# Optimization experiments

Measured on AMD Instinct MI355X. Metric: run time of the kernel, lower is better.

The kernel has to match this reference:

```python
import jax, jax.numpy as jnp
import numpy as np

N_NODES = 100000
N_EDGES = 3200000
N_GRAPHS = 64
NUM_CLASSES = 40


def _pointnet_layer(h, pos, src, dst, w1, b1, w2, b2):
    # message: mlp(concat([h_j, pos_j - pos_i])) for each edge (j=src, i=dst)
    edge_feat = jnp.concatenate([h[src], pos[src] - pos[dst]], axis=-1)  # [E, Cin+3]
    m = jnp.maximum(edge_feat @ w1 + b1, 0.0) @ w2 + b2                  # [E, Cout]
    # scatter-max aggregation to destination nodes
    agg = jax.ops.segment_max(m, dst, num_segments=N_NODES)             # [N, Cout]
    # nodes with no incoming edges get -inf from segment_max; PyG fills 0
    return jnp.where(jnp.isfinite(agg), agg, 0.0)


def setup_inputs() -> dict:
    key = jax.random.key(0)
    ks = jax.random.split(key, 12)
    pos = jax.random.normal(ks[0], (N_NODES, 3), dtype=jnp.float32)
    edge_index = jax.random.randint(ks[1], (2, N_EDGES), 0, N_NODES, dtype=jnp.int64 if jax.config.jax_enable_x64 else jnp.int32)
    batch = jnp.sort(jax.random.randint(ks[2], (N_NODES,), 0, N_GRAPHS, dtype=jnp.int32))
    s = 0.1
    params = {
        'w1a': jax.random.normal(ks[3], (6, 32), dtype=jnp.float32) * s,
        'b1a': jnp.zeros((32,), dtype=jnp.float32),
        'w2a': jax.random.normal(ks[4], (32, 32), dtype=jnp.float32) * s,
        'b2a': jnp.zeros((32,), dtype=jnp.float32),
        'w1b': jax.random.normal(ks[5], (35, 32), dtype=jnp.float32) * s,
        'b1b': jnp.zeros((32,), dtype=jnp.float32),
        'w2b': jax.random.normal(ks[6], (32, 32), dtype=jnp.float32) * s,
        'b2b': jnp.zeros((32,), dtype=jnp.float32),
        'wc': jax.random.normal(ks[7], (32, NUM_CLASSES), dtype=jnp.float32) * s,
        'bc': jnp.zeros((NUM_CLASSES,), dtype=jnp.float32),
    }
    return {'pos': pos, 'edge_index': edge_index, 'batch': batch, **params}


def reference(pos, edge_index, batch, w1a, b1a, w2a, b2a, w1b, b1b, w2b, b2b, wc, bc):
    src, dst = edge_index[0], edge_index[1]
    h = _pointnet_layer(pos, pos, src, dst, w1a, b1a, w2a, b2a)  # conv1: 3 -> 32
    h = jnp.maximum(h, 0.0)
    h = _pointnet_layer(h, pos, src, dst, w1b, b1b, w2b, b2b)    # conv2: 32 -> 32
    h = jnp.maximum(h, 0.0)
    g = jax.ops.segment_max(h, batch, num_segments=N_GRAPHS)     # global max pool [G, 32]
    g = jnp.where(jnp.isfinite(g), g, 0.0)
    return g @ wc + bc                                           # [G, num_classes]
```

## Files before the change

### kernel.cpp

```cpp
#include <hip/hip_runtime.h>
#include <hip/hip_fp16.h>

#define N_NODES 100000
#define N_EDGES 3200000
#define N_GRAPHS 64
#define NUM_CLASSES 40
#define DEG_BINS 512


__global__ void hist_kernel(const int* __restrict__ dst, int* __restrict__ cnt, int n_edges) {
    int idx = blockIdx.x * blockDim.x + threadIdx.x;
    int stride = gridDim.x * blockDim.x;
    for (int e = idx; e < n_edges; e += stride)
        atomicAdd(&cnt[dst[e]], 1);
}

__global__ __launch_bounds__(1024) void scan_kernel(int* __restrict__ cnt_cursor,
                                                    int* __restrict__ row_start,
                                                    int n_nodes) {
    const int T = 1024;
    int t = threadIdx.x;
    int chunk = (n_nodes + T - 1) / T;
    int s = t * chunk;
    int e = min(s + chunk, n_nodes);
    int sum = 0;
    for (int i = s; i < e; ++i) sum += cnt_cursor[i];
    __shared__ int tmp[T];
    tmp[t] = sum;
    __syncthreads();
    for (int off = 1; off < T; off <<= 1) {
        int v = (t >= off) ? tmp[t - off] : 0;
        __syncthreads();
        tmp[t] += v;
        __syncthreads();
    }
    int run = tmp[t] - sum;
    for (int i = s; i < e; ++i) {
        int c = cnt_cursor[i];
        row_start[i] = run;
        cnt_cursor[i] = run;
        run += c;
    }
    if (t == T - 1) row_start[n_nodes] = run;
}

__global__ void scatter_kernel(const int* __restrict__ src, const int* __restrict__ dst,
                               int* __restrict__ cursor, int* __restrict__ col, int n_edges) {
    int idx = blockIdx.x * blockDim.x + threadIdx.x;
    int stride = gridDim.x * blockDim.x;
    for (int e = idx; e < n_edges; e += stride) {
        int p = atomicAdd(&cursor[dst[e]], 1);
        col[p] = src[e];
    }
}


__global__ void deg_hist_kernel(const int* __restrict__ row_start, int* __restrict__ dhist,
                                int n_nodes) {
    int n = blockIdx.x * blockDim.x + threadIdx.x;
    if (n >= n_nodes) return;
    int d = row_start[n + 1] - row_start[n];
    atomicAdd(&dhist[min(d, DEG_BINS - 1)], 1);
}

__global__ __launch_bounds__(DEG_BINS) void deg_scan_kernel(const int* __restrict__ dhist,
                                                            int* __restrict__ dcur) {
    __shared__ int tmp[DEG_BINS];
    int t = threadIdx.x;
    int v = dhist[t];
    tmp[t] = v;
    __syncthreads();
    for (int off = 1; off < DEG_BINS; off <<= 1) {
        int u = (t >= off) ? tmp[t - off] : 0;
        __syncthreads();
        tmp[t] += u;
        __syncthreads();
    }
    dcur[t] = tmp[t] - v;
}

__global__ void deg_perm_kernel(const int* __restrict__ row_start, int* __restrict__ dcur,
                                int* __restrict__ perm, int n_nodes) {
    int n = blockIdx.x * blockDim.x + threadIdx.x;
    if (n >= n_nodes) return;
    int d = row_start[n + 1] - row_start[n];
    int p = atomicAdd(&dcur[min(d, DEG_BINS - 1)], 1);
    perm[p] = n;
}


__global__ void pqa_kernel(const float* __restrict__ pos, const float* __restrict__ w1a,
                           const float* __restrict__ b1a,
                           __half* __restrict__ P, float* __restrict__ Q, int n_nodes) {
    __shared__ float wtop[3][32], wbot[3][32], sb1[32];
    int t = threadIdx.x;
    if (t < 32) {
        for (int c = 0; c < 3; ++c) {
            wtop[c][t] = w1a[c * 32 + t];
            wbot[c][t] = w1a[(3 + c) * 32 + t];
        }
        sb1[t] = b1a[t];
    }
    __syncthreads();
    int n = blockIdx.x * blockDim.x + t;
    if (n >= n_nodes) return;
    float px = pos[n * 3 + 0], py = pos[n * 3 + 1], pz = pos[n * 3 + 2];
    __attribute__((aligned(16))) __half hv[32];
    float qv[32];
#pragma unroll
    for (int k = 0; k < 32; ++k) {
        float wb = fmaf(px, wbot[0][k], fmaf(py, wbot[1][k], pz * wbot[2][k]));
        float wt = fmaf(px, wtop[0][k], fmaf(py, wtop[1][k], pz * wtop[2][k]));
        hv[k] = __float2half_rn(wt + wb);
        qv[k] = wb - sb1[k];
    }
    float4* Pp = (float4*)(P + (size_t)n * 32);
#pragma unroll
    for (int k = 0; k < 4; ++k) Pp[k] = *(float4*)&hv[k * 8];
    float4* Qp = (float4*)(Q + (size_t)n * 32);
#pragma unroll
    for (int k = 0; k < 8; ++k) Qp[k] = *(float4*)&qv[k * 4];
}

__global__ __launch_bounds__(256) void pqb_kernel(const float* __restrict__ pos,
                                                  const float* __restrict__ H,
                                                  const float* __restrict__ w1b,
                                                  const float* __restrict__ b1b,
                                                  __half* __restrict__ P, float* __restrict__ Q,
                                                  int n_nodes) {
    __shared__ float sw[35 * 32];
    __shared__ float sb1[32];
    for (int i = threadIdx.x; i < 35 * 32; i += blockDim.x) sw[i] = w1b[i];
    if (threadIdx.x < 32) sb1[threadIdx.x] = b1b[threadIdx.x];
    __syncthreads();
    int n = blockIdx.x * blockDim.x + threadIdx.x;
    if (n >= n_nodes) return;
    float h[32];
    const float4* Hp = (const float4*)(H + (size_t)n * 32);
#pragma unroll
    for (int k = 0; k < 8; ++k) *(float4*)&h[k * 4] = Hp[k];
    float px = pos[n * 3 + 0], py = pos[n * 3 + 1], pz = pos[n * 3 + 2];
    __attribute__((aligned(16))) __half hv[32];
    float qv[32];
#pragma unroll
    for (int k = 0; k < 32; ++k) {
        float pd = fmaf(px, sw[32 * 32 + k], fmaf(py, sw[33 * 32 + k], pz * sw[34 * 32 + k]));
        float hd = 0.f;
#pragma unroll
        for (int c = 0; c < 32; ++c) hd = fmaf(h[c], sw[c * 32 + k], hd);
        hv[k] = __float2half_rn(hd + pd);
        qv[k] = pd - sb1[k];
    }
    float4* Pp = (float4*)(P + (size_t)n * 32);
#pragma unroll
    for (int k = 0; k < 4; ++k) Pp[k] = *(float4*)&hv[k * 8];
    float4* Qp = (float4*)(Q + (size_t)n * 32);
#pragma unroll
    for (int k = 0; k < 8; ++k) Qp[k] = *(float4*)&qv[k * 4];
}


template <int S>
__device__ __forceinline__ float qb(float v) {
#if __has_builtin(__builtin_amdgcn_update_dpp)
    int iv = __float_as_int(v);
    return __int_as_float(
        __builtin_amdgcn_update_dpp(iv, iv, S * 0x55, 0xf, 0xf, false));
#else
    return __shfl(v, S, 4);
#endif
}

__device__ __forceinline__ void unpack8(float4 r, float* x) {
    const __half2* h = (const __half2*)&r;
    float2 f;
    f = __half22float2(h[0]); x[0] = f.x; x[1] = f.y;
    f = __half22float2(h[1]); x[2] = f.x; x[3] = f.y;
    f = __half22float2(h[2]); x[4] = f.x; x[5] = f.y;
    f = __half22float2(h[3]); x[6] = f.x; x[7] = f.y;
}

#define KBLOCK(S, FIRST)                                                       \
    _Pragma("unroll") for (int r = 0; r < 8; ++r) {                            \
        float wv[8];                                                           \
        const float* wr = sw2 + (S * 8 + r) * 32 + c8;                         \
        *(float4*)&wv[0] = *(const float4*)(wr);                               \
        *(float4*)&wv[4] = *(const float4*)(wr + 4);                           \
        float ya = qb<S>(xa[r]);                                               \
        float yb = qb<S>(xb[r]);                                               \
        float yc = qb<S>(xc[r]);                                               \
        float yd = qb<S>(xd[r]);                                               \
        if (FIRST && r == 0) {                                                 \
            _Pragma("unroll") for (int jl = 0; jl < 8; ++jl) {                 \
                ma[jl] = ya * wv[jl];                                          \
                mb[jl] = yb * wv[jl];                                          \
                mc[jl] = yc * wv[jl];                                          \
                md[jl] = yd * wv[jl];                                          \
            }                                                                  \
        } else {                                                               \
            _Pragma("unroll") for (int jl = 0; jl < 8; ++jl) {                 \
                ma[jl] = fmaf(ya, wv[jl], ma[jl]);                             \
                mb[jl] = fmaf(yb, wv[jl], mb[jl]);                             \
                mc[jl] = fmaf(yc, wv[jl], mc[jl]);                             \
                md[jl] = fmaf(yd, wv[jl], md[jl]);                             \
            }                                                                  \
        }                                                                      \
    }

__global__ __launch_bounds__(256, 4) void edge_kernel(const int* __restrict__ perm,
                                                      const int* __restrict__ row_start,
                                                      const int* __restrict__ col,
                                                      const __half* __restrict__ P,
                                                      const float* __restrict__ Q,
                                                      const float* __restrict__ w2,
                                                      const float* __restrict__ b2,
                                                      float* __restrict__ H, int n_nodes) {
    __shared__ float sw2[32 * 32];
    __shared__ float sb2[32];
    for (int i = threadIdx.x; i < 32 * 32; i += blockDim.x) sw2[i] = w2[i];
    if (threadIdx.x < 32) sb2[threadIdx.x] = b2[threadIdx.x];
    __syncthreads();
    int gid = (blockIdx.x * blockDim.x + threadIdx.x) >> 2;
    int c = threadIdx.x & 3;
    if (gid >= n_nodes) return;
    int n = perm[gid];
    int c8 = c * 8;

    float q[8];
    {
        const float4* Qp = (const float4*)(Q + (size_t)n * 32 + c8);
        *(float4*)&q[0] = Qp[0];
        *(float4*)&q[4] = Qp[1];
    }
    float acc[8];
#pragma unroll
    for (int j = 0; j < 8; ++j) acc[j] = -3.0e38f;

    int e0 = row_start[n], e1 = row_start[n + 1];
    for (int e = e0; e < e1; e += 4) {
        int el = e1 - 1;
        int ia = col[e];
        int ib = col[min(e + 1, el)];
        int ic = col[min(e + 2, el)];
        int id = col[min(e + 3, el)];
        float4 ra = *(const float4*)(P + (size_t)ia * 32 + c8);
        float4 rb = *(const float4*)(P + (size_t)ib * 32 + c8);
        float4 rc = *(const float4*)(P + (size_t)ic * 32 + c8);
        float4 rd = *(const float4*)(P + (size_t)id * 32 + c8);
        float xa[8], xb[8], xc[8], xd[8];
        unpack8(ra, xa);
        unpack8(rb, xb);
        unpack8(rc, xc);
        unpack8(rd, xd);
#pragma unroll
        for (int r = 0; r < 8; ++r) {
            xa[r] = fmaxf(xa[r] - q[r], 0.f);
            xb[r] = fmaxf(xb[r] - q[r], 0.f);
            xc[r] = fmaxf(xc[r] - q[r], 0.f);
            xd[r] = fmaxf(xd[r] - q[r], 0.f);
        }
        float ma[8], mb[8], mc[8], md[8];
        KBLOCK(0, true)
        KBLOCK(1, false)
        KBLOCK(2, false)
        KBLOCK(3, false)
#pragma unroll
        for (int jl = 0; jl < 8; ++jl)
            acc[jl] = fmaxf(acc[jl], fmaxf(fmaxf(ma[jl], mb[jl]), fmaxf(mc[jl], md[jl])));
    }
    float outv[8];
#pragma unroll
    for (int jl = 0; jl < 8; ++jl) outv[jl] = fmaxf(acc[jl] + sb2[c8 + jl], 0.f);
    float4* Hp = (float4*)(H + (size_t)n * 32 + c8);
    Hp[0] = *(float4*)&outv[0];
    Hp[1] = *(float4*)&outv[4];
}

__global__ __launch_bounds__(256) void pool_kernel(const float* __restrict__ H,
                                                   const int* __restrict__ batch,
                                                   float* __restrict__ gmax, int n_nodes) {
    int g = blockIdx.x;
    int lo = 0, hi = n_nodes;
    while (lo < hi) { int mid = (lo + hi) >> 1; if (batch[mid] < g) lo = mid + 1; else hi = mid; }
    int s = lo;
    lo = 0; hi = n_nodes;
    while (lo < hi) { int mid = (lo + hi) >> 1; if (batch[mid] < g + 1) lo = mid + 1; else hi = mid; }
    int e = lo;

    float acc[32];
#pragma unroll
    for (int ch = 0; ch < 32; ++ch) acc[ch] = 0.f;
    for (int n = s + threadIdx.x; n < e; n += blockDim.x) {
        const float4* Hp = (const float4*)(H + (size_t)n * 32);
#pragma unroll
        for (int k = 0; k < 8; ++k) {
            float4 v = Hp[k];
            acc[k * 4 + 0] = fmaxf(acc[k * 4 + 0], v.x);
            acc[k * 4 + 1] = fmaxf(acc[k * 4 + 1], v.y);
            acc[k * 4 + 2] = fmaxf(acc[k * 4 + 2], v.z);
            acc[k * 4 + 3] = fmaxf(acc[k * 4 + 3], v.w);
        }
    }
#pragma unroll
    for (int off = 32; off >= 1; off >>= 1)
#pragma unroll
        for (int ch = 0; ch < 32; ++ch) acc[ch] = fmaxf(acc[ch], __shfl_xor(acc[ch], off));
    __shared__ float red[4][32];
    int wid = threadIdx.x >> 6, lane = threadIdx.x & 63;
    if (lane == 0)
#pragma unroll
        for (int ch = 0; ch < 32; ++ch) red[wid][ch] = acc[ch];
    __syncthreads();
    if (threadIdx.x < 32) {
        int ch = threadIdx.x;
        float v = fmaxf(fmaxf(red[0][ch], red[1][ch]), fmaxf(red[2][ch], red[3][ch]));
        gmax[g * 32 + ch] = v;
    }
}

__global__ void classifier_kernel(const float* __restrict__ gmax, const float* __restrict__ wc,
                                  const float* __restrict__ bc, float* __restrict__ out) {
    int idx = blockIdx.x * blockDim.x + threadIdx.x;
    if (idx >= N_GRAPHS * NUM_CLASSES) return;
    int g = idx / NUM_CLASSES, c = idx % NUM_CLASSES;
    float v = bc[c];
#pragma unroll
    for (int k = 0; k < 32; ++k) v = fmaf(gmax[g * 32 + k], wc[k * NUM_CLASSES + c], v);
    out[idx] = v;
}


extern "C" void kernel_launch(void* const* d_in, const int* in_sizes, int n_in,
                              void* d_out, int out_size, void* d_ws, size_t ws_size,
                              hipStream_t stream) {
    const float* pos = (const float*)d_in[0];
    const int* ei = (const int*)d_in[1];
    const int* batch = (const int*)d_in[2];
    const float* w1a = (const float*)d_in[3];
    const float* b1a = (const float*)d_in[4];
    const float* w2a = (const float*)d_in[5];
    const float* b2a = (const float*)d_in[6];
    const float* w1b = (const float*)d_in[7];
    const float* b1b = (const float*)d_in[8];
    const float* w2b = (const float*)d_in[9];
    const float* b2b = (const float*)d_in[10];
    const float* wc = (const float*)d_in[11];
    const float* bc = (const float*)d_in[12];
    float* out = (float*)d_out;

    __half* Pbuf = (__half*)d_ws;
    float* Qbuf = (float*)d_ws + (size_t)N_NODES * 32;
    float* Hbuf = Qbuf + (size_t)N_NODES * 32;
    int* row_start = (int*)(Hbuf + (size_t)N_NODES * 32);
    int* cursor = row_start + (N_NODES + 1);
    int* col = cursor + N_NODES;
    int* perm = col + N_EDGES;
    int* dhist = perm + N_NODES;
    int* dcur = dhist + DEG_BINS;
    float* gmax = (float*)(dcur + DEG_BINS);

    const int* srcv = ei;
    const int* dstv = ei + N_EDGES;

    hipMemsetAsync(cursor, 0, N_NODES * sizeof(int), stream);
    hipMemsetAsync(dhist, 0, DEG_BINS * sizeof(int), stream);
    hist_kernel<<<2048, 256, 0, stream>>>(dstv, cursor, N_EDGES);
    scan_kernel<<<1, 1024, 0, stream>>>(cursor, row_start, N_NODES);
    scatter_kernel<<<2048, 256, 0, stream>>>(srcv, dstv, cursor, col, N_EDGES);

    int nblk = (N_NODES + 255) / 256;
    deg_hist_kernel<<<nblk, 256, 0, stream>>>(row_start, dhist, N_NODES);
    deg_scan_kernel<<<1, DEG_BINS, 0, stream>>>(dhist, dcur);
    deg_perm_kernel<<<nblk, 256, 0, stream>>>(row_start, dcur, perm, N_NODES);

    int eblk = ((N_NODES * 4) + 255) / 256;
    pqa_kernel<<<nblk, 256, 0, stream>>>(pos, w1a, b1a, Pbuf, Qbuf, N_NODES);
    edge_kernel<<<eblk, 256, 0, stream>>>(perm, row_start, col, Pbuf, Qbuf, w2a, b2a, Hbuf, N_NODES);
    pqb_kernel<<<nblk, 256, 0, stream>>>(pos, Hbuf, w1b, b1b, Pbuf, Qbuf, N_NODES);
    edge_kernel<<<eblk, 256, 0, stream>>>(perm, row_start, col, Pbuf, Qbuf, w2b, b2b, Hbuf, N_NODES);

    pool_kernel<<<N_GRAPHS, 256, 0, stream>>>(Hbuf, batch, gmax, N_NODES);
    classifier_kernel<<<(N_GRAPHS * NUM_CLASSES + 255) / 256, 256, 0, stream>>>(gmax, wc, bc, out);
}
```

Before: 2.621 ms.

## Shard edges by source range so edge gathers hit a cache-sized slice of P

Edges are bucketed into four shards by source-node range, giving a CSR per (shard, dst). Each edge-kernel block handles one shard, so its gathers of P rows come from a quarter of the node table and should get better cache locality. Per-shard partial maxima are written in fp16 and merged by a new reduce kernel that also adds the bias and applies the ReLU. The per-node Q term is now computed inside the edge kernel from pos, removing the Q buffer, in exchange for extra partial-max traffic, an extra launch, a four-times-larger scan, and fp16 rounding of the partial maxima.

```diff
diff --git a/kernel.cpp b/kernel.cpp
--- a/kernel.cpp
+++ b/kernel.cpp
@@ -6,23 +6,28 @@
 #define N_GRAPHS 64
 #define NUM_CLASSES 40
 #define DEG_BINS 512
-
-
-__global__ void hist_kernel(const int* __restrict__ dst, int* __restrict__ cnt, int n_edges) {
+#define NSH 4
+#define SHARD_N 25000
+
+
+__global__ void hist_kernel(const int* __restrict__ src, const int* __restrict__ dst,
+                            int* __restrict__ cnt, int n_edges) {
     int idx = blockIdx.x * blockDim.x + threadIdx.x;
     int stride = gridDim.x * blockDim.x;
-    for (int e = idx; e < n_edges; e += stride)
-        atomicAdd(&cnt[dst[e]], 1);
+    for (int e = idx; e < n_edges; e += stride) {
+        int s = src[e];
+        atomicAdd(&cnt[(s / SHARD_N) * N_NODES + dst[e]], 1);
+    }
 }
 
 __global__ __launch_bounds__(1024) void scan_kernel(int* __restrict__ cnt_cursor,
                                                     int* __restrict__ row_start,
-                                                    int n_nodes) {
+                                                    int n) {
     const int T = 1024;
     int t = threadIdx.x;
-    int chunk = (n_nodes + T - 1) / T;
+    int chunk = (n + T - 1) / T;
     int s = t * chunk;
-    int e = min(s + chunk, n_nodes);
+    int e = min(s + chunk, n);
     int sum = 0;
     for (int i = s; i < e; ++i) sum += cnt_cursor[i];
     __shared__ int tmp[T];
@@ -41,7 +46,7 @@
         cnt_cursor[i] = run;
         run += c;
     }
-    if (t == T - 1) row_start[n_nodes] = run;
+    if (t == T - 1) row_start[n] = run;
 }
 
 __global__ void scatter_kernel(const int* __restrict__ src, const int* __restrict__ dst,
@@ -49,18 +54,25 @@
     int idx = blockIdx.x * blockDim.x + threadIdx.x;
     int stride = gridDim.x * blockDim.x;
     for (int e = idx; e < n_edges; e += stride) {
-        int p = atomicAdd(&cursor[dst[e]], 1);
-        col[p] = src[e];
-    }
-}
-
-
-__global__ void deg_hist_kernel(const int* __restrict__ row_start, int* __restrict__ dhist,
+        int s = src[e];
+        int p = atomicAdd(&cursor[(s / SHARD_N) * N_NODES + dst[e]], 1);
+        col[p] = s;
+    }
+}
+
+
+__device__ __forceinline__ int total_deg(const int* rs, int n) {
+    int d = 0;
+#pragma unroll
+    for (int t = 0; t < NSH; ++t) d += rs[t * N_NODES + n + 1] - rs[t * N_NODES + n];
+    return d;
+}
+
+__global__ void deg_hist_kernel(const int* __restrict__ rs, int* __restrict__ dhist,
                                 int n_nodes) {
     int n = blockIdx.x * blockDim.x + threadIdx.x;
     if (n >= n_nodes) return;
-    int d = row_start[n + 1] - row_start[n];
-    atomicAdd(&dhist[min(d, DEG_BINS - 1)], 1);
+    atomicAdd(&dhist[min(total_deg(rs, n), DEG_BINS - 1)], 1);
 }
 
 __global__ __launch_bounds__(DEG_BINS) void deg_scan_kernel(const int* __restrict__ dhist,
@@ -79,59 +91,40 @@
     dcur[t] = tmp[t] - v;
 }
 
-__global__ void deg_perm_kernel(const int* __restrict__ row_start, int* __restrict__ dcur,
+__global__ void deg_perm_kernel(const int* __restrict__ rs, int* __restrict__ dcur,
                                 int* __restrict__ perm, int n_nodes) {
     int n = blockIdx.x * blockDim.x + threadIdx.x;
     if (n >= n_nodes) return;
-    int d = row_start[n + 1] - row_start[n];
-    int p = atomicAdd(&dcur[min(d, DEG_BINS - 1)], 1);
+    int p = atomicAdd(&dcur[min(total_deg(rs, n), DEG_BINS - 1)], 1);
     perm[p] = n;
 }
 
 
 __global__ void pqa_kernel(const float* __restrict__ pos, const float* __restrict__ w1a,
-                           const float* __restrict__ b1a,
-                           __half* __restrict__ P, float* __restrict__ Q, int n_nodes) {
-    __shared__ float wtop[3][32], wbot[3][32], sb1[32];
+                           __half* __restrict__ P, int n_nodes) {
+    __shared__ float wsum[3][32];
     int t = threadIdx.x;
-    if (t < 32) {
-        for (int c = 0; c < 3; ++c) {
-            wtop[c][t] = w1a[c * 32 + t];
-            wbot[c][t] = w1a[(3 + c) * 32 + t];
-        }
-        sb1[t] = b1a[t];
-    }
+    if (t < 32)
+        for (int c = 0; c < 3; ++c) wsum[c][t] = w1a[c * 32 + t] + w1a[(3 + c) * 32 + t];
     __syncthreads();
     int n = blockIdx.x * blockDim.x + t;
     if (n >= n_nodes) return;
     float px = pos[n * 3 + 0], py = pos[n * 3 + 1], pz = pos[n * 3 + 2];
     __attribute__((aligned(16))) __half hv[32];
-    float qv[32];
-#pragma unroll
-    for (int k = 0; k < 32; ++k) {
-        float wb = fmaf(px, wbot[0][k], fmaf(py, wbot[1][k], pz * wbot[2][k]));
-        float wt = fmaf(px, wtop[0][k], fmaf(py, wtop[1][k], pz * wtop[2][k]));
-        hv[k] = __float2half_rn(wt + wb);
-        qv[k] = wb - sb1[k];
-    }
+#pragma unroll
+    for (int k = 0; k < 32; ++k)
+        hv[k] = __float2half_rn(fmaf(px, wsum[0][k], fmaf(py, wsum[1][k], pz * wsum[2][k])));
     float4* Pp = (float4*)(P + (size_t)n * 32);
 #pragma unroll
     for (int k = 0; k < 4; ++k) Pp[k] = *(float4*)&hv[k * 8];
-    float4* Qp = (float4*)(Q + (size_t)n * 32);
-#pragma unroll
-    for (int k = 0; k < 8; ++k) Qp[k] = *(float4*)&qv[k * 4];
 }
 
 __global__ __launch_bounds__(256) void pqb_kernel(const float* __restrict__ pos,
                                                   const float* __restrict__ H,
                                                   const float* __restrict__ w1b,
-                                                  const float* __restrict__ b1b,
-                                                  __half* __restrict__ P, float* __restrict__ Q,
-                                                  int n_nodes) {
+                                                  __half* __restrict__ P, int n_nodes) {
     __shared__ float sw[35 * 32];
-    __shared__ float sb1[32];
     for (int i = threadIdx.x; i < 35 * 32; i += blockDim.x) sw[i] = w1b[i];
-    if (threadIdx.x < 32) sb1[threadIdx.x] = b1b[threadIdx.x];
     __syncthreads();
     int n = blockIdx.x * blockDim.x + threadIdx.x;
     if (n >= n_nodes) return;
@@ -141,7 +134,6 @@
     for (int k = 0; k < 8; ++k) *(float4*)&h[k * 4] = Hp[k];
     float px = pos[n * 3 + 0], py = pos[n * 3 + 1], pz = pos[n * 3 + 2];
     __attribute__((aligned(16))) __half hv[32];
-    float qv[32];
 #pragma unroll
     for (int k = 0; k < 32; ++k) {
         float pd = fmaf(px, sw[32 * 32 + k], fmaf(py, sw[33 * 32 + k], pz * sw[34 * 32 + k]));
@@ -149,14 +141,10 @@
 #pragma unroll
         for (int c = 0; c < 32; ++c) hd = fmaf(h[c], sw[c * 32 + k], hd);
         hv[k] = __float2half_rn(hd + pd);
-        qv[k] = pd - sb1[k];
     }
     float4* Pp = (float4*)(P + (size_t)n * 32);
 #pragma unroll
     for (int k = 0; k < 4; ++k) Pp[k] = *(float4*)&hv[k * 8];
-    float4* Qp = (float4*)(Q + (size_t)n * 32);
-#pragma unroll
-    for (int k = 0; k < 8; ++k) Qp[k] = *(float4*)&qv[k * 4];
 }
 
 
@@ -208,35 +196,45 @@
     }
 
 __global__ __launch_bounds__(256, 4) void edge_kernel(const int* __restrict__ perm,
-                                                      const int* __restrict__ row_start,
+                                                      const int* __restrict__ rs,
                                                       const int* __restrict__ col,
                                                       const __half* __restrict__ P,
-                                                      const float* __restrict__ Q,
+                                                      const float* __restrict__ pos,
+                                                      const float* __restrict__ wbot,
+                                                      const float* __restrict__ b1,
                                                       const float* __restrict__ w2,
-                                                      const float* __restrict__ b2,
-                                                      float* __restrict__ H, int n_nodes) {
+                                                      __half* __restrict__ pmax,
+                                                      int n_nodes) {
     __shared__ float sw2[32 * 32];
-    __shared__ float sb2[32];
+    __shared__ float swb[3][32];
+    __shared__ float sb1[32];
     for (int i = threadIdx.x; i < 32 * 32; i += blockDim.x) sw2[i] = w2[i];
-    if (threadIdx.x < 32) sb2[threadIdx.x] = b2[threadIdx.x];
-    __syncthreads();
-    int gid = (blockIdx.x * blockDim.x + threadIdx.x) >> 2;
+    if (threadIdx.x < 32) {
+        for (int c = 0; c < 3; ++c) swb[c][threadIdx.x] = wbot[c * 32 + threadIdx.x];
+        sb1[threadIdx.x] = b1[threadIdx.x];
+    }
+    __syncthreads();
+    int shard = blockIdx.x & (NSH - 1);
+    int chunk = blockIdx.x >> 2;
+    int gid = chunk * 64 + (threadIdx.x >> 2);
     int c = threadIdx.x & 3;
     if (gid >= n_nodes) return;
     int n = perm[gid];
     int c8 = c * 8;
 
+    float px = pos[n * 3 + 0], py = pos[n * 3 + 1], pz = pos[n * 3 + 2];
     float q[8];
-    {
-        const float4* Qp = (const float4*)(Q + (size_t)n * 32 + c8);
-        *(float4*)&q[0] = Qp[0];
-        *(float4*)&q[4] = Qp[1];
-    }
+#pragma unroll
+    for (int j = 0; j < 8; ++j)
+        q[j] = fmaf(px, swb[0][c8 + j], fmaf(py, swb[1][c8 + j], pz * swb[2][c8 + j])) -
+               sb1[c8 + j];
+
     float acc[8];
 #pragma unroll
     for (int j = 0; j < 8; ++j) acc[j] = -3.0e38f;
 
-    int e0 = row_start[n], e1 = row_start[n + 1];
+    int base = shard * N_NODES + n;
+    int e0 = rs[base], e1 = rs[base + 1];
     for (int e = e0; e < e1; e += 4) {
         int el = e1 - 1;
         int ia = col[e];
@@ -268,9 +266,33 @@
         for (int jl = 0; jl < 8; ++jl)
             acc[jl] = fmaxf(acc[jl], fmaxf(fmaxf(ma[jl], mb[jl]), fmaxf(mc[jl], md[jl])));
     }
+    __attribute__((aligned(16))) __half hv[8];
+#pragma unroll
+    for (int jl = 0; jl < 8; ++jl) hv[jl] = __float2half_rn(acc[jl]);
+    *(float4*)(pmax + (size_t)base * 32 + c8) = *(float4*)&hv[0];
+}
+
+__global__ __launch_bounds__(256) void reduce_kernel(const __half* __restrict__ pmax,
+                                                     const float* __restrict__ b2,
+                                                     float* __restrict__ H, int n_nodes) {
+    int idx = blockIdx.x * blockDim.x + threadIdx.x;
+    if (idx >= n_nodes * 4) return;
+    int n = idx >> 2, c = idx & 3;
+    int c8 = c * 8;
+    float m[8];
+#pragma unroll
+    for (int j = 0; j < 8; ++j) m[j] = -3.0e38f;
+#pragma unroll
+    for (int s = 0; s < NSH; ++s) {
+        float4 r = *(const float4*)(pmax + ((size_t)s * N_NODES + n) * 32 + c8);
+        float x[8];
+        unpack8(r, x);
+#pragma unroll
+        for (int j = 0; j < 8; ++j) m[j] = fmaxf(m[j], x[j]);
+    }
     float outv[8];
 #pragma unroll
-    for (int jl = 0; jl < 8; ++jl) outv[jl] = fmaxf(acc[jl] + sb2[c8 + jl], 0.f);
+    for (int j = 0; j < 8; ++j) outv[j] = fmaxf(m[j] + b2[c8 + j], 0.f);
     float4* Hp = (float4*)(H + (size_t)n * 32 + c8);
     Hp[0] = *(float4*)&outv[0];
     Hp[1] = *(float4*)&outv[4];
@@ -349,11 +371,11 @@
     float* out = (float*)d_out;
 
     __half* Pbuf = (__half*)d_ws;
-    float* Qbuf = (float*)d_ws + (size_t)N_NODES * 32;
-    float* Hbuf = Qbuf + (size_t)N_NODES * 32;
-    int* row_start = (int*)(Hbuf + (size_t)N_NODES * 32);
-    int* cursor = row_start + (N_NODES + 1);
-    int* col = cursor + N_NODES;
+    float* Hbuf = (float*)((char*)d_ws + (size_t)N_NODES * 32 * 2);
+    __half* pmax = (__half*)(Hbuf + (size_t)N_NODES * 32);
+    int* rs = (int*)(pmax + (size_t)NSH * N_NODES * 32);
+    int* cursor = rs + (NSH * N_NODES + 1);
+    int* col = cursor + NSH * N_NODES;
     int* perm = col + N_EDGES;
     int* dhist = perm + N_NODES;
     int* dcur = dhist + DEG_BINS;
@@ -362,22 +384,30 @@
     const int* srcv = ei;
     const int* dstv = ei + N_EDGES;
 
-    hipMemsetAsync(cursor, 0, N_NODES * sizeof(int), stream);
+    hipMemsetAsync(cursor, 0, NSH * N_NODES * sizeof(int), stream);
     hipMemsetAsync(dhist, 0, DEG_BINS * sizeof(int), stream);
-    hist_kernel<<<2048, 256, 0, stream>>>(dstv, cursor, N_EDGES);
-    scan_kernel<<<1, 1024, 0, stream>>>(cursor, row_start, N_NODES);
+    hist_kernel<<<2048, 256, 0, stream>>>(srcv, dstv, cursor, N_EDGES);
+    scan_kernel<<<1, 1024, 0, stream>>>(cursor, rs, NSH * N_NODES);
     scatter_kernel<<<2048, 256, 0, stream>>>(srcv, dstv, cursor, col, N_EDGES);
 
     int nblk = (N_NODES + 255) / 256;
-    deg_hist_kernel<<<nblk, 256, 0, stream>>>(row_start, dhist, N_NODES);
+    deg_hist_kernel<<<nblk, 256, 0, stream>>>(rs, dhist, N_NODES);
     deg_scan_kernel<<<1, DEG_BINS, 0, stream>>>(dhist, dcur);
-    deg_perm_kernel<<<nblk, 256, 0, stream>>>(row_start, dcur, perm, N_NODES);
-
-    int eblk = ((N_NODES * 4) + 255) / 256;
-    pqa_kernel<<<nblk, 256, 0, stream>>>(pos, w1a, b1a, Pbuf, Qbuf, N_NODES);
-    edge_kernel<<<eblk, 256, 0, stream>>>(perm, row_start, col, Pbuf, Qbuf, w2a, b2a, Hbuf, N_NODES);
-    pqb_kernel<<<nblk, 256, 0, stream>>>(pos, Hbuf, w1b, b1b, Pbuf, Qbuf, N_NODES);
-    edge_kernel<<<eblk, 256, 0, stream>>>(perm, row_start, col, Pbuf, Qbuf, w2b, b2b, Hbuf, N_NODES);
+    deg_perm_kernel<<<nblk, 256, 0, stream>>>(rs, dcur, perm, N_NODES);
+
+    int chunks = (N_NODES + 63) / 64;
+    int eblk = chunks * NSH;
+    int rblk = (N_NODES * 4 + 255) / 256;
+
+    pqa_kernel<<<nblk, 256, 0, stream>>>(pos, w1a, Pbuf, N_NODES);
+    edge_kernel<<<eblk, 256, 0, stream>>>(perm, rs, col, Pbuf, pos, w1a + 3 * 32, b1a, w2a,
+                                          pmax, N_NODES);
+    reduce_kernel<<<rblk, 256, 0, stream>>>(pmax, b2a, Hbuf, N_NODES);
+
+    pqb_kernel<<<nblk, 256, 0, stream>>>(pos, Hbuf, w1b, Pbuf, N_NODES);
+    edge_kernel<<<eblk, 256, 0, stream>>>(perm, rs, col, Pbuf, pos, w1b + 32 * 32, b1b, w2b,
+                                          pmax, N_NODES);
+    reduce_kernel<<<rblk, 256, 0, stream>>>(pmax, b2b, Hbuf, N_NODES);
 
     pool_kernel<<<N_GRAPHS, 256, 0, stream>>>(Hbuf, batch, gmax, N_NODES);
     classifier_kernel<<<(N_GRAPHS * NUM_CLASSES + 255) / 256, 256, 0, stream>>>(gmax, wc, bc, out);
```

Measured after the change: 4.341 ms. +65.6%, slower.
